# Kernel optimization log

Hardware: AMD Instinct MI355X
Metric: run time of the kernel (lower is better)

## Reference

```python
import jax, jax.numpy as jnp
import numpy as np

B, D, H, W, C = 2, 5, 32, 32, 256
NH, NL, NP = 8, 5, 16
HD = C // NH
MLP_H = 4 * C
HW = H * W
LQ = D * HW


def setup_inputs() -> dict:
    key = jax.random.key(0)
    ks = jax.random.split(key, 12)
    s = 0.02
    return {
        "x": jax.random.normal(ks[0], (B, D, H, W, C), jnp.float32),
        "reference_points": jax.random.uniform(ks[1], (B, LQ, NL, 2), jnp.float32),
        "spatial_shapes": np.array([[H, W]] * NL, np.int32),
        "level_start_index": (np.arange(NL) * HW).astype(np.int32),
        "norm3_g": jnp.ones((C,), jnp.float32),
        "norm3_b": jnp.zeros((C,), jnp.float32),
        "norm4_g": jnp.ones((C,), jnp.float32),
        "norm4_b": jnp.zeros((C,), jnp.float32),
        "w_off": jax.random.normal(ks[2], (C, NH * NL * NP * 2), jnp.float32) * s,
        "b_off": jnp.zeros((NH * NL * NP * 2,), jnp.float32),
        "w_attn": jax.random.normal(ks[3], (C, NH * NL * NP), jnp.float32) * s,
        "b_attn": jnp.zeros((NH * NL * NP,), jnp.float32),
        "w_val": jax.random.normal(ks[4], (C, C), jnp.float32) * s,
        "b_val": jnp.zeros((C,), jnp.float32),
        "w_out": jax.random.normal(ks[5], (C, C), jnp.float32) * s,
        "b_out": jnp.zeros((C,), jnp.float32),
        "w_fc1": jax.random.normal(ks[6], (C, MLP_H), jnp.float32) * s,
        "b_fc1": jnp.zeros((MLP_H,), jnp.float32),
        "w_fc2": jax.random.normal(ks[7], (MLP_H, C), jnp.float32) * s,
        "b_fc2": jnp.zeros((C,), jnp.float32),
    }


def _ln(x, g, b, eps=1e-5):
    m = x.mean(-1, keepdims=True)
    v = ((x - m) ** 2).mean(-1, keepdims=True)
    return (x - m) * jax.lax.rsqrt(v + eps) * g + b


def _msdeform(q, ref, w_off, b_off, w_attn, b_attn, w_val, b_val, w_out, b_out):
    """Standard Deformable-DETR MSDeformAttn; self-attention (value = query input)."""
    Bq = q.shape[0]
    val = (q @ w_val + b_val).reshape(Bq, LQ, NH, HD)
    off = (q @ w_off + b_off).reshape(Bq, LQ, NH, NL, NP, 2)
    aw = jax.nn.softmax((q @ w_attn + b_attn).reshape(Bq, LQ, NH, NL * NP), axis=-1)
    aw = aw.reshape(Bq, LQ, NH, NL, NP)
    # offset normalizer: (W, H) per level (all levels HxW here)
    loc = ref[:, :, None, :, None, :] + off / jnp.array([W, H], jnp.float32)
    out = jnp.zeros((Bq, LQ, NH, HD), jnp.float32)
    for l in range(NL):  # loop over 5 levels (structural, small)
        vl = val[:, l * HW:(l + 1) * HW].transpose(0, 2, 1, 3).reshape(Bq * NH, HW, HD)
        ll = loc[:, :, :, l].transpose(0, 2, 1, 3, 4)  # [B, NH, LQ, NP, 2]
        # grid_sample align_corners=False, grid = 2*loc - 1 => pixel = loc*size - 0.5
        px = ll[..., 0] * W - 0.5
        py = ll[..., 1] * H - 0.5
        x0 = jnp.floor(px)
        y0 = jnp.floor(py)
        fx = px - x0
        fy = py - y0
        x0i = x0.astype(jnp.int32)
        y0i = y0.astype(jnp.int32)
        samp = jnp.zeros((Bq * NH, LQ * NP, HD), jnp.float32)
        for dy, dx, wgt in ((0, 0, (1 - fy) * (1 - fx)), (0, 1, (1 - fy) * fx),
                            (1, 0, fy * (1 - fx)), (1, 1, fy * fx)):
            xi = x0i + dx
            yi = y0i + dy
            valid = ((xi >= 0) & (xi < W) & (yi >= 0) & (yi < H)).astype(jnp.float32)
            idx = (jnp.clip(yi, 0, H - 1) * W + jnp.clip(xi, 0, W - 1)).reshape(Bq * NH, LQ * NP, 1)
            g = jnp.take_along_axis(vl, idx, axis=1)  # [B*NH, LQ*NP, HD]
            samp = samp + g * (wgt * valid).reshape(Bq * NH, LQ * NP, 1)
        samp = samp.reshape(Bq, NH, LQ, NP, HD)
        out = out + jnp.einsum('bqhp,bhqpd->bqhd', aw[:, :, :, l], samp)
    return out.reshape(Bq, LQ, C) @ w_out + b_out


def reference(x, reference_points, spatial_shapes, level_start_index,
              norm3_g, norm3_b, norm4_g, norm4_b,
              w_off, b_off, w_attn, b_attn, w_val, b_val, w_out, b_out,
              w_fc1, b_fc1, w_fc2, b_fc2):
    # forward_part3: norm3 -> flatten -> MSDeformAttn (D == 5, no padding path)
    q = _ln(x, norm3_g, norm3_b).reshape(B, LQ, C)
    attn = _msdeform(q, reference_points, w_off, b_off, w_attn, b_attn,
                     w_val, b_val, w_out, b_out)
    x = x + attn.reshape(B, D, H, W, C)  # shortcut + drop_path(identity)
    # forward_part4: norm4 -> MLP (GELU, exact) residual
    h = _ln(x, norm4_g, norm4_b)
    m = jax.nn.gelu(h @ w_fc1 + b_fc1, approximate=False) @ w_fc2 + b_fc2
    return x + m
```

## Files before the change

### kernel.cpp

```cpp
#include <hip/hip_runtime.h>
#include <hip/hip_bf16.h>
#include <math.h>

#define B_   2
#define D_   5
#define H_   32
#define W_   32
#define C_   256
#define NH_  8
#define NL_  5
#define NP_  16
#define HD_  32
#define HW_  1024
#define LQ_  5120
#define M_   (B_*LQ_)
#define MLP_ 1024
#define NCAT 2176
#define NQ2  1920

typedef unsigned short u16;
typedef __bf16 bf16x8 __attribute__((ext_vector_type(8)));
typedef float  f32x4  __attribute__((ext_vector_type(4)));

__device__ __forceinline__ float b2f(u16 v) {
    union { float f; unsigned u; } x; x.u = ((unsigned)v) << 16; return x.f;
}
__device__ __forceinline__ u16 f2b(float f) {
    union { float f; unsigned u; } x; x.f = f;
    unsigned r = x.u + 0x7fffu + ((x.u >> 16) & 1u);
    return (u16)(r >> 16);
}
__device__ __forceinline__ void gload16(const u16* g, u16* l) {
    __builtin_amdgcn_global_load_lds(
        (const __attribute__((address_space(1))) unsigned int*)g,
        (__attribute__((address_space(3))) unsigned int*)l, 16, 0, 0);
}

#define SEG0 557056
#define SEG1 622592
#define SEG2 884736
#define SEG3 1146880
#define SEGT 1149056
__global__ void prep_weights(const float* __restrict__ w_val, const float* __restrict__ w_off,
                             const float* __restrict__ w_attn, const float* __restrict__ w_out,
                             const float* __restrict__ w_fc1, const float* __restrict__ w_fc2,
                             const float* __restrict__ b_val, const float* __restrict__ b_off,
                             const float* __restrict__ b_attn,
                             u16* __restrict__ wcatT, u16* __restrict__ woutT,
                             u16* __restrict__ wfc1T, u16* __restrict__ wfc2T,
                             float* __restrict__ biascat) {
    int idx = blockIdx.x * blockDim.x + threadIdx.x;
    if (idx < SEG0) {
        int n = idx >> 8, k = idx & 255;
        float v;
        if (n < 256)        v = w_val[k * 256 + n];
        else if (n < 1536)  v = w_off[k * 1280 + (n - 256)];
        else                v = w_attn[k * 640 + (n - 1536)];
        wcatT[idx] = f2b(v);
    } else if (idx < SEG1) {
        int i = idx - SEG0; int n = i >> 8, k = i & 255;
        woutT[i] = f2b(w_out[k * 256 + n]);
    } else if (idx < SEG2) {
        int i = idx - SEG1; int n = i >> 8, k = i & 255;
        wfc1T[i] = f2b(w_fc1[k * 1024 + n]);
    } else if (idx < SEG3) {
        int i = idx - SEG2; int n = i >> 10, k = i & 1023;
        wfc2T[i] = f2b(w_fc2[k * 256 + n]);
    } else if (idx < SEGT) {
        int t = idx - SEG3;
        float v;
        if (t < 256)        v = b_val[t];
        else if (t < 1536)  v = b_off[t - 256];
        else                v = b_attn[t - 1536];
        biascat[t] = v;
    }
}

__global__ void ln_rows(const float* __restrict__ x, const float* __restrict__ g,
                        const float* __restrict__ b, u16* __restrict__ out) {
    int wave = threadIdx.x >> 6, lane = threadIdx.x & 63;
    int row = blockIdx.x * 4 + wave;
    const float4 v = *(const float4*)(x + (size_t)row * C_ + lane * 4);
    float s = v.x + v.y + v.z + v.w;
#pragma unroll
    for (int o = 1; o < 64; o <<= 1) s += __shfl_xor(s, o, 64);
    float mean = s * (1.0f / C_);
    float4 d = { v.x - mean, v.y - mean, v.z - mean, v.w - mean };
    float s2 = d.x * d.x + d.y * d.y + d.z * d.z + d.w * d.w;
#pragma unroll
    for (int o = 1; o < 64; o <<= 1) s2 += __shfl_xor(s2, o, 64);
    float r = rsqrtf(s2 * (1.0f / C_) + 1e-5f);
    const float4 gg = *(const float4*)(g + lane * 4);
    const float4 bb = *(const float4*)(b + lane * 4);
    unsigned lo = (unsigned)f2b(d.x * r * gg.x + bb.x) |
                  ((unsigned)f2b(d.y * r * gg.y + bb.y) << 16);
    unsigned hi = (unsigned)f2b(d.z * r * gg.z + bb.z) |
                  ((unsigned)f2b(d.w * r * gg.w + bb.w) << 16);
    uint2 pk = { lo, hi };
    *(uint2*)(out + (size_t)row * C_ + lane * 4) = pk;
}

#define BK 64
__launch_bounds__(256, 2)
__global__ void gemm128(const u16* __restrict__ A, const u16* __restrict__ Bt,
                        const float* __restrict__ bias,
                        u16* __restrict__ out, u16* __restrict__ valT,
                        int Mdim, int Ndim, int Kdim,
                        int mode, int nTiles) {
    __shared__ __align__(16) u16 lsA[128 * BK];
    __shared__ __align__(16) u16 lsB[128 * BK];
    int bm = blockIdx.x / nTiles, bn = blockIdx.x % nTiles;
    int m0 = bm * 128, n0 = bn * 128;
    int tid = threadIdx.x;
    int lane = tid & 63, wv = tid >> 6;
    int quad = lane >> 4, l16 = lane & 15;
    int rw = (wv >> 1) * 64, cw = (wv & 1) * 64;

    f32x4 acc[4][4];
#pragma unroll
    for (int i = 0; i < 4; i++)
#pragma unroll
        for (int j = 0; j < 4; j++) { f32x4 z = {0.f, 0.f, 0.f, 0.f}; acc[i][j] = z; }

    for (int k0 = 0; k0 < Kdim; k0 += BK) {
        __syncthreads();
#pragma unroll
        for (int s = 0; s < 4; s++) {
            int cc = s * 256 + wv * 64 + lane;
            int row = cc >> 3, kc = (cc & 7) << 3;
            int lbase = (s * 256 + wv * 64) * 8;
            gload16(A  + (size_t)(m0 + row) * Kdim + k0 + kc, &lsA[lbase]);
            gload16(Bt + (size_t)(n0 + row) * Kdim + k0 + kc, &lsB[lbase]);
        }
        __syncthreads();
#pragma unroll
        for (int kk = 0; kk < 2; kk++) {
            bf16x8 af[4], bfr[4];
#pragma unroll
            for (int i = 0; i < 4; i++)
                af[i] = *(const bf16x8*)(&lsA[(rw + i * 16 + l16) * BK + kk * 32 + quad * 8]);
#pragma unroll
            for (int j = 0; j < 4; j++)
                bfr[j] = *(const bf16x8*)(&lsB[(cw + j * 16 + l16) * BK + kk * 32 + quad * 8]);
#pragma unroll
            for (int i = 0; i < 4; i++)
#pragma unroll
                for (int j = 0; j < 4; j++)
                    acc[i][j] = __builtin_amdgcn_mfma_f32_16x16x32_bf16(
                        af[i], bfr[j], acc[i][j], 0, 0, 0);
        }
    }

#pragma unroll
    for (int i = 0; i < 4; i++) {
#pragma unroll
        for (int j = 0; j < 4; j++) {
            int col = n0 + cw + j * 16 + l16;
            float bb = bias[col];
#pragma unroll
            for (int r = 0; r < 4; r++) {
                int row = m0 + rw + i * 16 + quad * 4 + r;
                float v = acc[i][j][r] + bb;
                if (mode == 0) {
                    if (col < 256) {
                        int b2 = row >= LQ_;
                        int pix = row - b2 * LQ_;
                        int h = col >> 5, ch = col & 31;
                        valT[(((size_t)(b2 * NH_ + h) * LQ_) + pix) * 32 + ch] = f2b(v);
                    } else {
                        out[(size_t)row * NQ2 + (col - 256)] = f2b(v);
                    }
                } else {
                    float t = 0.5f * v * (1.0f + erff(v * 0.70710678f));
                    out[(size_t)row * Ndim + col] = f2b(t);
                }
            }
        }
    }
}

__launch_bounds__(256, 2)
__global__ void gemm_wout_ln(const u16* __restrict__ A, const u16* __restrict__ Bt,
                             const float* __restrict__ bias, const float* __restrict__ res,
                             const float* __restrict__ g4, const float* __restrict__ b4,
                             float* __restrict__ x2, u16* __restrict__ hb) {
    __shared__ __align__(16) u16 lsA[32 * BK];
    __shared__ __align__(16) u16 lsB[256 * BK];
    int m0 = blockIdx.x * 32;
    int tid = threadIdx.x;
    int lane = tid & 63, wv = tid >> 6;
    int quad = lane >> 4, l16 = lane & 15;
    int r0 = (wv & 1) * 16, c0 = (wv >> 1) * 128;

    f32x4 acc[8];
#pragma unroll
    for (int j = 0; j < 8; j++) { f32x4 z = {0.f, 0.f, 0.f, 0.f}; acc[j] = z; }

    for (int k0 = 0; k0 < 256; k0 += BK) {
        __syncthreads();
        {
            int cc = wv * 64 + lane;
            int row = cc >> 3, kc = (cc & 7) << 3;
            gload16(A + (size_t)(m0 + row) * 256 + k0 + kc, &lsA[(wv * 64) * 8]);
        }
#pragma unroll
        for (int s = 0; s < 8; s++) {
            int cc = s * 256 + wv * 64 + lane;
            int row = cc >> 3, kc = (cc & 7) << 3;
            gload16(Bt + (size_t)row * 256 + k0 + kc, &lsB[(s * 256 + wv * 64) * 8]);
        }
        __syncthreads();
#pragma unroll
        for (int kk = 0; kk < 2; kk++) {
            bf16x8 af, bfr[8];
            af = *(const bf16x8*)(&lsA[(r0 + l16) * BK + kk * 32 + quad * 8]);
#pragma unroll
            for (int j = 0; j < 8; j++)
                bfr[j] = *(const bf16x8*)(&lsB[(c0 + j * 16 + l16) * BK + kk * 32 + quad * 8]);
#pragma unroll
            for (int j = 0; j < 8; j++)
                acc[j] = __builtin_amdgcn_mfma_f32_16x16x32_bf16(af, bfr[j], acc[j], 0, 0, 0);
        }
    }

    __syncthreads();
    float* tile = (float*)lsB;
#pragma unroll
    for (int j = 0; j < 8; j++) {
        int col = c0 + j * 16 + l16;
        float bb = bias[col];
#pragma unroll
        for (int r = 0; r < 4; r++) {
            int rl = r0 + quad * 4 + r;
            int row = m0 + rl;
            float v = acc[j][r] + bb + res[(size_t)row * C_ + col];
            tile[rl * 256 + col] = v;
            x2[(size_t)row * C_ + col] = v;
        }
    }
    __syncthreads();
    const float4 gg = *(const float4*)(g4 + lane * 4);
    const float4 bv = *(const float4*)(b4 + lane * 4);
#pragma unroll
    for (int rr = 0; rr < 8; rr++) {
        int rl = wv * 8 + rr;
        float4 v = *(const float4*)(&tile[rl * 256 + lane * 4]);
        float s = v.x + v.y + v.z + v.w;
        float s2 = v.x * v.x + v.y * v.y + v.z * v.z + v.w * v.w;
#pragma unroll
        for (int o = 1; o < 64; o <<= 1) {
            s  += __shfl_xor(s, o, 64);
            s2 += __shfl_xor(s2, o, 64);
        }
        float mean = s * (1.0f / C_);
        float var = s2 * (1.0f / C_) - mean * mean;
        float rstd = rsqrtf(var + 1e-5f);
        unsigned lo = (unsigned)f2b((v.x - mean) * rstd * gg.x + bv.x) |
                      ((unsigned)f2b((v.y - mean) * rstd * gg.y + bv.y) << 16);
        unsigned hi = (unsigned)f2b((v.z - mean) * rstd * gg.z + bv.z) |
                      ((unsigned)f2b((v.w - mean) * rstd * gg.w + bv.w) << 16);
        uint2 pk = { lo, hi };
        *(uint2*)(hb + (size_t)(m0 + rl) * C_ + lane * 4) = pk;
    }
}

__launch_bounds__(256, 4)
__global__ void gemm64_res(const u16* __restrict__ A, const u16* __restrict__ Bt,
                           const float* __restrict__ bias, const float* __restrict__ res,
                           float* __restrict__ out, int Mdim, int Ndim, int Kdim,
                           int nTiles) {
    __shared__ __align__(16) u16 lsA[64 * BK];
    __shared__ __align__(16) u16 lsB[128 * BK];
    int bm = blockIdx.x / nTiles, bn = blockIdx.x % nTiles;
    int m0 = bm * 64, n0 = bn * 128;
    int tid = threadIdx.x;
    int lane = tid & 63, wv = tid >> 6;
    int quad = lane >> 4, l16 = lane & 15;
    int rw = wv * 16;

    f32x4 acc[8];
#pragma unroll
    for (int j = 0; j < 8; j++) { f32x4 z = {0.f, 0.f, 0.f, 0.f}; acc[j] = z; }

    for (int k0 = 0; k0 < Kdim; k0 += BK) {
        __syncthreads();
#pragma unroll
        for (int s = 0; s < 2; s++) {
            int cc = s * 256 + wv * 64 + lane;
            int row = cc >> 3, kc = (cc & 7) << 3;
            gload16(A + (size_t)(m0 + row) * Kdim + k0 + kc, &lsA[(s * 256 + wv * 64) * 8]);
        }
#pragma unroll
        for (int s = 0; s < 4; s++) {
            int cc = s * 256 + wv * 64 + lane;
            int row = cc >> 3, kc = (cc & 7) << 3;
            gload16(Bt + (size_t)(n0 + row) * Kdim + k0 + kc, &lsB[(s * 256 + wv * 64) * 8]);
        }
        __syncthreads();
#pragma unroll
        for (int kk = 0; kk < 2; kk++) {
            bf16x8 af, bfr[8];
            af = *(const bf16x8*)(&lsA[(rw + l16) * BK + kk * 32 + quad * 8]);
#pragma unroll
            for (int j = 0; j < 8; j++)
                bfr[j] = *(const bf16x8*)(&lsB[(j * 16 + l16) * BK + kk * 32 + quad * 8]);
#pragma unroll
            for (int j = 0; j < 8; j++)
                acc[j] = __builtin_amdgcn_mfma_f32_16x16x32_bf16(af, bfr[j], acc[j], 0, 0, 0);
        }
    }

#pragma unroll
    for (int j = 0; j < 8; j++) {
        int col = n0 + j * 16 + l16;
        float bb = bias[col];
#pragma unroll
        for (int r = 0; r < 4; r++) {
            int row = m0 + rw + quad * 4 + r;
            size_t off = (size_t)row * Ndim + col;
            out[off] = acc[j][r] + bb + res[off];
        }
    }
}

#define SPC 84
__launch_bounds__(256, 2)
__global__ void msdeform_sample(const u16* __restrict__ qkv2,
                                const u16* __restrict__ valT,
                                const float* __restrict__ ref,
                                u16* __restrict__ outp) {
    __shared__ int2 sparam[NH_ * 4 * SPC];
    int m = blockIdx.x;
    int b = m / LQ_;
    int tid = threadIdx.x;
    int g = tid >> 5;
    int lane = tid & 31;

    const u16* logit_base = qkv2 + (size_t)m * NQ2 + 1280 + g * 80;
    const u16* off_base   = qkv2 + (size_t)m * NQ2 + g * 160;

    float lv[3];
    float lmax = -1e30f;
    {
        int c = 0;
        for (int i = lane; i < 80; i += 32, c++) {
            lv[c] = b2f(logit_base[i]);
            lmax = fmaxf(lmax, lv[c]);
        }
    }
#pragma unroll
    for (int o = 16; o > 0; o >>= 1) lmax = fmaxf(lmax, __shfl_xor(lmax, o, 32));
    float lsum = 0.f;
    {
        int c = 0;
        for (int i = lane; i < 80; i += 32, c++) {
            lv[c] = __expf(lv[c] - lmax);
            lsum += lv[c];
        }
    }
#pragma unroll
    for (int o = 16; o > 0; o >>= 1) lsum += __shfl_xor(lsum, o, 32);
    float inv = 1.0f / lsum;

    {
        int c = 0;
        for (int i = lane; i < 80; i += 32, c++) {
            float aw = lv[c] * inv;
            int l = i >> 4, p = i & 15;
            float rx = ref[((size_t)m * NL_ + l) * 2 + 0];
            float ry = ref[((size_t)m * NL_ + l) * 2 + 1];
            float ox = b2f(off_base[l * 32 + p * 2 + 0]);
            float oy = b2f(off_base[l * 32 + p * 2 + 1]);
            float px = rx * (float)W_ + ox - 0.5f;
            float py = ry * (float)H_ + oy - 0.5f;
            float x0 = floorf(px), y0 = floorf(py);
            float fx = px - x0, fy = py - y0;
            int x0i = (int)x0, y0i = (int)y0;
            int hbase = (b * NH_ + g) * LQ_ + l * HW_;
            int sbase = g * 4 * SPC + i;
#pragma unroll
            for (int cc = 0; cc < 4; cc++) {
                int dy = cc >> 1, dx = cc & 1;
                int xi = x0i + dx, yi = y0i + dy;
                float wgt = (dy ? fy : 1.f - fy) * (dx ? fx : 1.f - fx);
                bool valid = (xi >= 0) && (xi < W_) && (yi >= 0) && (yi < H_);
                int xc = min(max(xi, 0), W_ - 1);
                int yc = min(max(yi, 0), H_ - 1);
                int boff = (hbase + yc * W_ + xc) * 64;
                float w = valid ? wgt * aw : 0.f;
                int2 pk = { boff, __float_as_int(w) };
                sparam[sbase + cc * SPC] = pk;
            }
        }
    }
    __syncthreads();

    const char* qb = (const char*)valT;
    int c4 = lane >> 3;
    int s2 = (lane >> 2) & 1;
    int chq = lane & 3;
    int pbase = g * 4 * SPC + c4 * SPC + s2;
    int laneoff = chq * 16;
    float a0 = 0.f, a1 = 0.f, a2 = 0.f, a3 = 0.f;
    float a4 = 0.f, a5 = 0.f, a6 = 0.f, a7 = 0.f;
#pragma unroll 4
    for (int i = 0; i < 40; i++) {
        int2 p = sparam[pbase + i * 2];
        float w = __int_as_float(p.y);
        uint4 v = *(const uint4*)(qb + p.x + laneoff);
        union { unsigned u; float f; } t;
        t.u = v.x << 16;         a0 += w * t.f;
        t.u = v.x & 0xffff0000u; a1 += w * t.f;
        t.u = v.y << 16;         a2 += w * t.f;
        t.u = v.y & 0xffff0000u; a3 += w * t.f;
        t.u = v.z << 16;         a4 += w * t.f;
        t.u = v.z & 0xffff0000u; a5 += w * t.f;
        t.u = v.w << 16;         a6 += w * t.f;
        t.u = v.w & 0xffff0000u; a7 += w * t.f;
    }
#pragma unroll
    for (int o = 4; o <= 16; o <<= 1) {
        a0 += __shfl_xor(a0, o, 32); a1 += __shfl_xor(a1, o, 32);
        a2 += __shfl_xor(a2, o, 32); a3 += __shfl_xor(a3, o, 32);
        a4 += __shfl_xor(a4, o, 32); a5 += __shfl_xor(a5, o, 32);
        a6 += __shfl_xor(a6, o, 32); a7 += __shfl_xor(a7, o, 32);
    }
    if (lane < 4) {
        uint4 pk;
        pk.x = (unsigned)f2b(a0) | ((unsigned)f2b(a1) << 16);
        pk.y = (unsigned)f2b(a2) | ((unsigned)f2b(a3) << 16);
        pk.z = (unsigned)f2b(a4) | ((unsigned)f2b(a5) << 16);
        pk.w = (unsigned)f2b(a6) | ((unsigned)f2b(a7) << 16);
        *(uint4*)(outp + (size_t)m * C_ + g * 32 + chq * 8) = pk;
    }
}

extern "C" void kernel_launch(void* const* d_in, const int* in_sizes, int n_in,
                              void* d_out, int out_size, void* d_ws, size_t ws_size,
                              hipStream_t stream) {
    const float* x      = (const float*)d_in[0];
    const float* ref    = (const float*)d_in[1];
    const float* n3g    = (const float*)d_in[4];
    const float* n3b    = (const float*)d_in[5];
    const float* n4g    = (const float*)d_in[6];
    const float* n4b    = (const float*)d_in[7];
    const float* w_off  = (const float*)d_in[8];
    const float* b_off  = (const float*)d_in[9];
    const float* w_attn = (const float*)d_in[10];
    const float* b_attn = (const float*)d_in[11];
    const float* w_val  = (const float*)d_in[12];
    const float* b_val  = (const float*)d_in[13];
    const float* w_out  = (const float*)d_in[14];
    const float* b_out  = (const float*)d_in[15];
    const float* w_fc1  = (const float*)d_in[16];
    const float* b_fc1  = (const float*)d_in[17];
    const float* w_fc2  = (const float*)d_in[18];
    const float* b_fc2  = (const float*)d_in[19];
    float* out = (float*)d_out;

    u16*   wcatT   = (u16*)d_ws;
    float* biascat = (float*)(wcatT + (size_t)NCAT * 256);
    u16*   woutT   = (u16*)(biascat + 2304);
    u16*   wfc1T   = woutT + 256 * 256;
    u16*   wfc2T   = wfc1T + 1024 * 256;
    u16*   qbuf    = wfc2T + 256 * 1024;
    u16*   valT    = qbuf + (size_t)M_ * 256;
    u16*   qkv2    = valT + (size_t)M_ * 256;
    u16*   outp    = qkv2 + (size_t)M_ * NQ2;
    float* x2      = (float*)qkv2;
    u16*   hbuf    = (u16*)(x2 + (size_t)M_ * 256);
    u16*   gbuf    = hbuf + (size_t)M_ * 256;

    prep_weights<<<dim3((SEGT + 255) / 256), dim3(256), 0, stream>>>(
        w_val, w_off, w_attn, w_out, w_fc1, w_fc2, b_val, b_off, b_attn,
        wcatT, woutT, wfc1T, wfc2T, biascat);

    ln_rows<<<dim3(M_ / 4), dim3(256), 0, stream>>>(x, n3g, n3b, qbuf);

    gemm128<<<dim3(80 * 17), dim3(256), 0, stream>>>(
        qbuf, wcatT, biascat, qkv2, valT, M_, NCAT, 256, 0, 17);

    msdeform_sample<<<dim3(M_), dim3(256), 0, stream>>>(qkv2, valT, ref, outp);

    gemm_wout_ln<<<dim3(M_ / 32), dim3(256), 0, stream>>>(
        outp, woutT, b_out, x, n4g, n4b, x2, hbuf);

    gemm128<<<dim3(80 * 8), dim3(256), 0, stream>>>(
        hbuf, wfc1T, b_fc1, gbuf, nullptr, M_, 1024, 256, 1, 8);

    gemm64_res<<<dim3(160 * 2), dim3(256), 0, stream>>>(
        gbuf, wfc2T, b_fc2, x2, out, M_, 256, 1024, 2);
}
```

Before: 263.5 us.

## Splat bilinear weights into per-head LDS window grid and fuse prep with first LayerNorm

The deformable sampling kernel no longer gathers four corners for every sampling point. For each level it splats the bilinear weights into a per-head 8x8 LDS grid centred on the reference point, using LDS atomics. It then gathers each non-zero grid pixel once, so repeated corner fetches are deduplicated, and whole rows with no weight are skipped via a ballot. Corners that fall outside the window go to a small overflow list that is gathered separately. The weight-prep kernel and the norm3 LayerNorm kernel are also merged into one launch to save a kernel launch, at the cost of LDS atomics and branchy per-level work whose benefit depends on how concentrated the offsets are.

```diff
diff --git a/kernel.cpp b/kernel.cpp
--- a/kernel.cpp
+++ b/kernel.cpp
@@ -41,14 +41,40 @@
 #define SEG2 884736
 #define SEG3 1146880
 #define SEGT 1149056
-__global__ void prep_weights(const float* __restrict__ w_val, const float* __restrict__ w_off,
+#define PREP_BLKS ((SEGT + 255) / 256)
+__global__ void prep_and_ln3(const float* __restrict__ w_val, const float* __restrict__ w_off,
                              const float* __restrict__ w_attn, const float* __restrict__ w_out,
                              const float* __restrict__ w_fc1, const float* __restrict__ w_fc2,
                              const float* __restrict__ b_val, const float* __restrict__ b_off,
                              const float* __restrict__ b_attn,
                              u16* __restrict__ wcatT, u16* __restrict__ woutT,
                              u16* __restrict__ wfc1T, u16* __restrict__ wfc2T,
-                             float* __restrict__ biascat) {
+                             float* __restrict__ biascat,
+                             const float* __restrict__ x, const float* __restrict__ g3,
+                             const float* __restrict__ b3, u16* __restrict__ qbuf) {
+    if (blockIdx.x >= PREP_BLKS) {
+        int wave = threadIdx.x >> 6, lane = threadIdx.x & 63;
+        int row = (blockIdx.x - PREP_BLKS) * 4 + wave;
+        const float4 v = *(const float4*)(x + (size_t)row * C_ + lane * 4);
+        float s = v.x + v.y + v.z + v.w;
+#pragma unroll
+        for (int o = 1; o < 64; o <<= 1) s += __shfl_xor(s, o, 64);
+        float mean = s * (1.0f / C_);
+        float4 d = { v.x - mean, v.y - mean, v.z - mean, v.w - mean };
+        float s2 = d.x * d.x + d.y * d.y + d.z * d.z + d.w * d.w;
+#pragma unroll
+        for (int o = 1; o < 64; o <<= 1) s2 += __shfl_xor(s2, o, 64);
+        float r = rsqrtf(s2 * (1.0f / C_) + 1e-5f);
+        const float4 gg = *(const float4*)(g3 + lane * 4);
+        const float4 bb = *(const float4*)(b3 + lane * 4);
+        unsigned lo = (unsigned)f2b(d.x * r * gg.x + bb.x) |
+                      ((unsigned)f2b(d.y * r * gg.y + bb.y) << 16);
+        unsigned hi = (unsigned)f2b(d.z * r * gg.z + bb.z) |
+                      ((unsigned)f2b(d.w * r * gg.w + bb.w) << 16);
+        uint2 pk = { lo, hi };
+        *(uint2*)(qbuf + (size_t)row * C_ + lane * 4) = pk;
+        return;
+    }
     int idx = blockIdx.x * blockDim.x + threadIdx.x;
     if (idx < SEG0) {
         int n = idx >> 8, k = idx & 255;
@@ -76,30 +102,6 @@
     }
 }
 
-__global__ void ln_rows(const float* __restrict__ x, const float* __restrict__ g,
-                        const float* __restrict__ b, u16* __restrict__ out) {
-    int wave = threadIdx.x >> 6, lane = threadIdx.x & 63;
-    int row = blockIdx.x * 4 + wave;
-    const float4 v = *(const float4*)(x + (size_t)row * C_ + lane * 4);
-    float s = v.x + v.y + v.z + v.w;
-#pragma unroll
-    for (int o = 1; o < 64; o <<= 1) s += __shfl_xor(s, o, 64);
-    float mean = s * (1.0f / C_);
-    float4 d = { v.x - mean, v.y - mean, v.z - mean, v.w - mean };
-    float s2 = d.x * d.x + d.y * d.y + d.z * d.z + d.w * d.w;
-#pragma unroll
-    for (int o = 1; o < 64; o <<= 1) s2 += __shfl_xor(s2, o, 64);
-    float r = rsqrtf(s2 * (1.0f / C_) + 1e-5f);
-    const float4 gg = *(const float4*)(g + lane * 4);
-    const float4 bb = *(const float4*)(b + lane * 4);
-    unsigned lo = (unsigned)f2b(d.x * r * gg.x + bb.x) |
-                  ((unsigned)f2b(d.y * r * gg.y + bb.y) << 16);
-    unsigned hi = (unsigned)f2b(d.z * r * gg.z + bb.z) |
-                  ((unsigned)f2b(d.w * r * gg.w + bb.w) << 16);
-    uint2 pk = { lo, hi };
-    *(uint2*)(out + (size_t)row * C_ + lane * 4) = pk;
-}
-
 #define BK 64
 __launch_bounds__(256, 2)
 __global__ void gemm128(const u16* __restrict__ A, const u16* __restrict__ Bt,
@@ -323,13 +325,15 @@
     }
 }
 
-#define SPC 84
+#define OVF_CAP 64
 __launch_bounds__(256, 2)
 __global__ void msdeform_sample(const u16* __restrict__ qkv2,
                                 const u16* __restrict__ valT,
                                 const float* __restrict__ ref,
                                 u16* __restrict__ outp) {
-    __shared__ int2 sparam[NH_ * 4 * SPC];
+    __shared__ float grid[NH_][64];
+    __shared__ int2  ovf[NH_][OVF_CAP];
+    __shared__ int   ovfcnt[NH_];
     int m = blockIdx.x;
     int b = m / LQ_;
     int tid = threadIdx.x;
@@ -339,13 +343,13 @@
     const u16* logit_base = qkv2 + (size_t)m * NQ2 + 1280 + g * 80;
     const u16* off_base   = qkv2 + (size_t)m * NQ2 + g * 160;
 
-    float lv[3];
+    float a80[3];
     float lmax = -1e30f;
     {
         int c = 0;
         for (int i = lane; i < 80; i += 32, c++) {
-            lv[c] = b2f(logit_base[i]);
-            lmax = fmaxf(lmax, lv[c]);
+            a80[c] = b2f(logit_base[i]);
+            lmax = fmaxf(lmax, a80[c]);
         }
     }
 #pragma unroll
@@ -354,83 +358,118 @@
     {
         int c = 0;
         for (int i = lane; i < 80; i += 32, c++) {
-            lv[c] = __expf(lv[c] - lmax);
-            lsum += lv[c];
+            a80[c] = __expf(a80[c] - lmax);
+            lsum += a80[c];
         }
     }
 #pragma unroll
     for (int o = 16; o > 0; o >>= 1) lsum += __shfl_xor(lsum, o, 32);
     float inv = 1.0f / lsum;
-
-    {
-        int c = 0;
-        for (int i = lane; i < 80; i += 32, c++) {
-            float aw = lv[c] * inv;
-            int l = i >> 4, p = i & 15;
-            float rx = ref[((size_t)m * NL_ + l) * 2 + 0];
-            float ry = ref[((size_t)m * NL_ + l) * 2 + 1];
-            float ox = b2f(off_base[l * 32 + p * 2 + 0]);
-            float oy = b2f(off_base[l * 32 + p * 2 + 1]);
-            float px = rx * (float)W_ + ox - 0.5f;
-            float py = ry * (float)H_ + oy - 0.5f;
+    a80[0] *= inv; a80[1] *= inv; a80[2] *= inv;
+
+    int pt = lane & 15, cp = lane >> 4;
+    int chq = lane & 3, cellpar = lane >> 2;
+    int hbase = (b * NH_ + g) * LQ_;
+    const char* vb = (const char*)valT;
+
+    float acc[8];
+#pragma unroll
+    for (int i = 0; i < 8; i++) acc[i] = 0.f;
+
+#pragma unroll
+    for (int l = 0; l < NL_; l++) {
+        grid[g][lane] = 0.f;
+        grid[g][lane + 32] = 0.f;
+        if (lane == 0) ovfcnt[g] = 0;
+
+        float rx = ref[((size_t)m * NL_ + l) * 2 + 0];
+        float ry = ref[((size_t)m * NL_ + l) * 2 + 1];
+        int wx0 = (int)floorf(rx * 32.f - 0.5f) - 3;
+        int wy0 = (int)floorf(ry * 32.f - 0.5f) - 3;
+
+        {
+            unsigned o2 = *(const unsigned*)(off_base + l * 32 + pt * 2);
+            float ox = b2f((u16)(o2 & 0xffffu));
+            float oy = b2f((u16)(o2 >> 16));
+            float aw = __shfl(a80[l >> 1], (l & 1) * 16 + pt, 32);
+            float px = rx * 32.f + ox - 0.5f;
+            float py = ry * 32.f + oy - 0.5f;
             float x0 = floorf(px), y0 = floorf(py);
             float fx = px - x0, fy = py - y0;
             int x0i = (int)x0, y0i = (int)y0;
-            int hbase = (b * NH_ + g) * LQ_ + l * HW_;
-            int sbase = g * 4 * SPC + i;
-#pragma unroll
-            for (int cc = 0; cc < 4; cc++) {
-                int dy = cc >> 1, dx = cc & 1;
-                int xi = x0i + dx, yi = y0i + dy;
-                float wgt = (dy ? fy : 1.f - fy) * (dx ? fx : 1.f - fx);
-                bool valid = (xi >= 0) && (xi < W_) && (yi >= 0) && (yi < H_);
-                int xc = min(max(xi, 0), W_ - 1);
-                int yc = min(max(yi, 0), H_ - 1);
-                int boff = (hbase + yc * W_ + xc) * 64;
-                float w = valid ? wgt * aw : 0.f;
-                int2 pk = { boff, __float_as_int(w) };
-                sparam[sbase + cc * SPC] = pk;
+            int yi = y0i + cp;
+            float wy = (cp ? fy : 1.f - fy) * aw;
+            bool yok = (yi >= 0) && (yi < H_);
+#pragma unroll
+            for (int dx = 0; dx < 2; dx++) {
+                int xi = x0i + dx;
+                float w = wy * (dx ? fx : 1.f - fx);
+                if (yok && xi >= 0 && xi < W_ && w != 0.f) {
+                    int cxx = xi - wx0, cyy = yi - wy0;
+                    if (((unsigned)cxx < 8u) && ((unsigned)cyy < 8u)) {
+                        atomicAdd(&grid[g][cyy * 8 + cxx], w);
+                    } else {
+                        int idx = atomicAdd(&ovfcnt[g], 1);
+                        int2 e = { hbase + l * HW_ + yi * W_ + xi, __float_as_int(w) };
+                        ovf[g][idx] = e;
+                    }
+                }
             }
         }
-    }
-    __syncthreads();
-
-    const char* qb = (const char*)valT;
-    int c4 = lane >> 3;
-    int s2 = (lane >> 2) & 1;
-    int chq = lane & 3;
-    int pbase = g * 4 * SPC + c4 * SPC + s2;
-    int laneoff = chq * 16;
-    float a0 = 0.f, a1 = 0.f, a2 = 0.f, a3 = 0.f;
-    float a4 = 0.f, a5 = 0.f, a6 = 0.f, a7 = 0.f;
-#pragma unroll 4
-    for (int i = 0; i < 40; i++) {
-        int2 p = sparam[pbase + i * 2];
-        float w = __int_as_float(p.y);
-        uint4 v = *(const uint4*)(qb + p.x + laneoff);
-        union { unsigned u; float f; } t;
-        t.u = v.x << 16;         a0 += w * t.f;
-        t.u = v.x & 0xffff0000u; a1 += w * t.f;
-        t.u = v.y << 16;         a2 += w * t.f;
-        t.u = v.y & 0xffff0000u; a3 += w * t.f;
-        t.u = v.z << 16;         a4 += w * t.f;
-        t.u = v.z & 0xffff0000u; a5 += w * t.f;
-        t.u = v.w << 16;         a6 += w * t.f;
-        t.u = v.w & 0xffff0000u; a7 += w * t.f;
-    }
+
+        int rowpix = hbase + l * HW_ + wy0 * W_ + wx0;
+#pragma unroll
+        for (int ryy = 0; ryy < 8; ryy++) {
+            float w = grid[g][ryy * 8 + cellpar];
+            if (__ballot(w != 0.f) == 0ull) continue;
+            if (w != 0.f) {
+                const char* p = vb + ((size_t)(unsigned)(rowpix + ryy * W_ + cellpar)) * 64 + chq * 16;
+                uint4 v = *(const uint4*)p;
+                union { unsigned u; float f; } t;
+                t.u = v.x << 16;         acc[0] += w * t.f;
+                t.u = v.x & 0xffff0000u; acc[1] += w * t.f;
+                t.u = v.y << 16;         acc[2] += w * t.f;
+                t.u = v.y & 0xffff0000u; acc[3] += w * t.f;
+                t.u = v.z << 16;         acc[4] += w * t.f;
+                t.u = v.z & 0xffff0000u; acc[5] += w * t.f;
+                t.u = v.w << 16;         acc[6] += w * t.f;
+                t.u = v.w & 0xffff0000u; acc[7] += w * t.f;
+            }
+        }
+
+        int n = ovfcnt[g];
+        for (int i = 0; i < n; i++) {
+            int2 e = ovf[g][i];
+            if (cellpar == 0) {
+                float w = __int_as_float(e.y);
+                const char* p = vb + (size_t)(unsigned)e.x * 64 + chq * 16;
+                uint4 v = *(const uint4*)p;
+                union { unsigned u; float f; } t;
+                t.u = v.x << 16;         acc[0] += w * t.f;
+                t.u = v.x & 0xffff0000u; acc[1] += w * t.f;
+                t.u = v.y << 16;         acc[2] += w * t.f;
+                t.u = v.y & 0xffff0000u; acc[3] += w * t.f;
+                t.u = v.z << 16;         acc[4] += w * t.f;
+                t.u = v.z & 0xffff0000u; acc[5] += w * t.f;
+                t.u = v.w << 16;         acc[6] += w * t.f;
+                t.u = v.w & 0xffff0000u; acc[7] += w * t.f;
+            }
+        }
+    }
+
 #pragma unroll
     for (int o = 4; o <= 16; o <<= 1) {
-        a0 += __shfl_xor(a0, o, 32); a1 += __shfl_xor(a1, o, 32);
-        a2 += __shfl_xor(a2, o, 32); a3 += __shfl_xor(a3, o, 32);
-        a4 += __shfl_xor(a4, o, 32); a5 += __shfl_xor(a5, o, 32);
-        a6 += __shfl_xor(a6, o, 32); a7 += __shfl_xor(a7, o, 32);
+        acc[0] += __shfl_xor(acc[0], o, 32); acc[1] += __shfl_xor(acc[1], o, 32);
+        acc[2] += __shfl_xor(acc[2], o, 32); acc[3] += __shfl_xor(acc[3], o, 32);
+        acc[4] += __shfl_xor(acc[4], o, 32); acc[5] += __shfl_xor(acc[5], o, 32);
+        acc[6] += __shfl_xor(acc[6], o, 32); acc[7] += __shfl_xor(acc[7], o, 32);
     }
     if (lane < 4) {
         uint4 pk;
-        pk.x = (unsigned)f2b(a0) | ((unsigned)f2b(a1) << 16);
-        pk.y = (unsigned)f2b(a2) | ((unsigned)f2b(a3) << 16);
-        pk.z = (unsigned)f2b(a4) | ((unsigned)f2b(a5) << 16);
-        pk.w = (unsigned)f2b(a6) | ((unsigned)f2b(a7) << 16);
+        pk.x = (unsigned)f2b(acc[0]) | ((unsigned)f2b(acc[1]) << 16);
+        pk.y = (unsigned)f2b(acc[2]) | ((unsigned)f2b(acc[3]) << 16);
+        pk.z = (unsigned)f2b(acc[4]) | ((unsigned)f2b(acc[5]) << 16);
+        pk.w = (unsigned)f2b(acc[6]) | ((unsigned)f2b(acc[7]) << 16);
         *(uint4*)(outp + (size_t)m * C_ + g * 32 + chq * 8) = pk;
     }
 }
@@ -471,11 +510,9 @@
     u16*   hbuf    = (u16*)(x2 + (size_t)M_ * 256);
     u16*   gbuf    = hbuf + (size_t)M_ * 256;
 
-    prep_weights<<<dim3((SEGT + 255) / 256), dim3(256), 0, stream>>>(
+    prep_and_ln3<<<dim3(PREP_BLKS + M_ / 4), dim3(256), 0, stream>>>(
         w_val, w_off, w_attn, w_out, w_fc1, w_fc2, b_val, b_off, b_attn,
-        wcatT, woutT, wfc1T, wfc2T, biascat);
-
-    ln_rows<<<dim3(M_ / 4), dim3(256), 0, stream>>>(x, n3g, n3b, qbuf);
+        wcatT, woutT, wfc1T, wfc2T, biascat, x, n3g, n3b, qbuf);
 
     gemm128<<<dim3(80 * 17), dim3(256), 0, stream>>>(
         qbuf, wcatT, biascat, qkv2, valT, M_, NCAT, 256, 0, 17);
```

Result: slower. 373.0 us (+41.6%).
